# Optimization experiments

Measured on AMD Instinct MI355X. Metric: run time of the kernel, lower is better.

Reference implementation:

```python
import jax, jax.numpy as jnp
import numpy as np

NUM_EXPERTS = 8
CAPACITY_C = 1.0
ROUTER_TEMP = 1.0
EPS = 1e-10


def reference(x, router_w, router_b, w_gate, b_gate, w_up, b_up, w_down, b_down):
    # x: [B, S, H]
    B, S, H = x.shape
    n_tok = B * S
    k = int(n_tok * CAPACITY_C) // NUM_EXPERTS  # expert capacity (1024 here)

    xf = x.reshape(n_tok, H)  # (b s) h

    # Linear router (dropout p=0 -> identity), computed in float32 as in .float()
    clean_h = xf @ router_w + router_b  # [n_tok, E]

    # Gumbel noise (deterministic key stands in for torch.rand_like)
    u = jax.random.uniform(jax.random.key(42), clean_h.shape, dtype=clean_h.dtype)
    gumbel = -jnp.log(-jnp.log(u + EPS) + EPS)
    h = (clean_h + gumbel) / ROUTER_TEMP

    Sm = jax.nn.softmax(h, axis=-1)  # softmax over experts

    # top-k over the TOKEN dim (dim=0) per expert -> expert-choice routing
    Gt, idxt = jax.lax.top_k(Sm.T, k)  # [E, k]
    G = Gt.T            # [k, E] routing weights
    idx = idxt.T        # [k, E] chosen token indices

    # Gather routed tokens (replaces the one-hot einsum gather exactly:
    # top-k indices are distinct per expert, so one-hot matmul == take)
    toks = jnp.take(xf, idx, axis=0)  # [k, E, H]

    # Shared SwiGLU FFN (group_size=1 -> one expert instance reused E times)
    gate = jax.nn.silu(toks @ w_gate + b_gate)  # [k, E, dff]
    up = toks @ w_up + b_up                      # [k, E, dff]
    e_out = (gate * up) @ w_down + b_down        # [k, E, H]

    # Weight by G and scatter-add back to token positions, summed over experts
    weighted = G[..., None] * e_out              # [k, E, H]
    y = jnp.zeros_like(xf).at[idx.reshape(-1)].add(weighted.reshape(-1, H))
    return y.reshape(B, S, H)


def setup_inputs() -> dict:
    key = jax.random.key(0)
    ks = jax.random.split(key, 6)
    B, S, H, E = 4, 2048, 2048, NUM_EXPERTS
    dff = int(H * 4 * 2 / 3)  # 5461
    sH = 1.0 / np.sqrt(H)
    sF = 1.0 / np.sqrt(dff)
    return {
        "x": jax.random.normal(ks[0], (B, S, H), dtype=jnp.float32),
        "router_w": jax.random.normal(ks[1], (H, E), dtype=jnp.float32) * sH,
        "router_b": jnp.zeros((E,), dtype=jnp.float32),
        "w_gate": jax.random.normal(ks[2], (H, dff), dtype=jnp.float32) * sH,
        "b_gate": jnp.zeros((dff,), dtype=jnp.float32),
        "w_up": jax.random.normal(ks[3], (H, dff), dtype=jnp.float32) * sH,
        "b_up": jnp.zeros((dff,), dtype=jnp.float32),
        "w_down": jax.random.normal(ks[4], (dff, H), dtype=jnp.float32) * sF,
        "b_down": jnp.zeros((H,), dtype=jnp.float32),
    }
```

## Files before the change

kernel.cpp:

```cpp
#include <hip/hip_runtime.h>
#include <cstdint>
#include <cstddef>

#define N_TOK  8192
#define HDIM   2048
#define NEXP   8
#define KCAP   1024
#define DFF    5461
#define DFF_PB 5504
#define ACT_P  5504
#define NT1    (HDIM / 64)
#define NT2    (ACT_P / 64)

typedef unsigned short u16;
typedef short bf16x8 __attribute__((ext_vector_type(8)));
typedef float f32x4  __attribute__((ext_vector_type(4)));

__device__ __forceinline__ u16 f2bf(float f) {
  uint32_t u = __float_as_uint(f);
  uint32_t r = (u + 0x7FFFu + ((u >> 16) & 1u)) >> 16;
  return (u16)r;
}

__device__ __forceinline__ uint32_t rotl32(uint32_t v, int d) {
  return (v << d) | (v >> (32 - d));
}

__device__ uint32_t threefry_bits(uint32_t idx) {
  const uint32_t ks0 = 0u, ks1 = 42u, ks2 = 0u ^ 42u ^ 0x1BD11BDAu;
  uint32_t x0 = 0u + ks0;
  uint32_t x1 = idx + ks1;
#define TFR(d) { x0 += x1; x1 = rotl32(x1, d); x1 ^= x0; }
  TFR(13) TFR(15) TFR(26) TFR(6)
  x0 += ks1; x1 += ks2 + 1u;
  TFR(17) TFR(29) TFR(16) TFR(24)
  x0 += ks2; x1 += ks0 + 2u;
  TFR(13) TFR(15) TFR(26) TFR(6)
  x0 += ks0; x1 += ks1 + 3u;
  TFR(17) TFR(29) TFR(16) TFR(24)
  x0 += ks1; x1 += ks2 + 4u;
  TFR(13) TFR(15) TFR(26) TFR(6)
  x0 += ks2; x1 += ks0 + 5u;
#undef TFR
  return x0 ^ x1;
}

__global__ __launch_bounds__(256) void router_kernel(const float* __restrict__ x,
    const float* __restrict__ rw, const float* __restrict__ rb,
    float* __restrict__ SmT)
{
  const int lane = threadIdx.x & 63;
  const int wid  = threadIdx.x >> 6;
  const int t = blockIdx.x * 4 + wid;
  const float* xr = x + (size_t)t * HDIM;
  float acc[8] = {0.f,0.f,0.f,0.f,0.f,0.f,0.f,0.f};
#pragma unroll
  for (int it = 0; it < HDIM / 64; ++it) {
    int h = lane + it * 64;
    float xv = xr[h];
    const float4* wp = (const float4*)(rw + h * 8);
    float4 w0 = wp[0], w1 = wp[1];
    acc[0] = fmaf(xv, w0.x, acc[0]);
    acc[1] = fmaf(xv, w0.y, acc[1]);
    acc[2] = fmaf(xv, w0.z, acc[2]);
    acc[3] = fmaf(xv, w0.w, acc[3]);
    acc[4] = fmaf(xv, w1.x, acc[4]);
    acc[5] = fmaf(xv, w1.y, acc[5]);
    acc[6] = fmaf(xv, w1.z, acc[6]);
    acc[7] = fmaf(xv, w1.w, acc[7]);
  }
#pragma unroll
  for (int m = 32; m >= 1; m >>= 1) {
#pragma unroll
    for (int e = 0; e < 8; ++e) acc[e] += __shfl_xor(acc[e], m, 64);
  }
  if (lane == 0) {
    float h[8];
#pragma unroll
    for (int e = 0; e < 8; ++e) {
      uint32_t bits = threefry_bits((uint32_t)(t * 8 + e));
      float u = __uint_as_float((bits >> 9) | 0x3f800000u) - 1.0f;
      u = fmaxf(u, 0.0f);
      float g = -logf(-logf(u + 1e-10f) + 1e-10f);
      h[e] = acc[e] + rb[e] + g;
    }
    float mx = h[0];
#pragma unroll
    for (int e = 1; e < 8; ++e) mx = fmaxf(mx, h[e]);
    float ex[8]; float s = 0.f;
#pragma unroll
    for (int e = 0; e < 8; ++e) { ex[e] = expf(h[e] - mx); s += ex[e]; }
#pragma unroll
    for (int e = 0; e < 8; ++e) SmT[e * N_TOK + t] = ex[e] / s;
  }
}

__global__ __launch_bounds__(1024) void select_topk(const float* __restrict__ SmT,
    uint32_t* __restrict__ selTok, float* __restrict__ selW)
{
  const int e = blockIdx.x;
  const int tid = threadIdx.x;
  const float* v = SmT + (size_t)e * N_TOK;
  __shared__ uint32_t hist[256];
  __shared__ uint32_t sh_byte, sh_kk, sh_cnt, sh_eqc;
  uint32_t bitsv[8];
#pragma unroll
  for (int i = 0; i < 8; ++i) bitsv[i] = __float_as_uint(v[tid + i * 1024]);
  uint32_t prefix = 0;
  uint32_t kk = KCAP;
  for (int s = 3; s >= 0; --s) {
    if (tid < 256) hist[tid] = 0;
    __syncthreads();
    uint32_t himask = (s == 3) ? 0u : (0xFFFFFFFFu << ((s + 1) * 8));
#pragma unroll
    for (int i = 0; i < 8; ++i) {
      uint32_t b = bitsv[i];
      if ((b & himask) == prefix) atomicAdd(&hist[(b >> (s * 8)) & 255u], 1u);
    }
    __syncthreads();
    if (tid == 0) {
      uint32_t cum = 0; uint32_t bsel = 0, kn = kk;
      for (int b = 255; b >= 0; --b) {
        uint32_t c = hist[b];
        if (cum + c >= kk) { bsel = (uint32_t)b; kn = kk - cum; break; }
        cum += c;
      }
      sh_byte = bsel; sh_kk = kn;
    }
    __syncthreads();
    prefix |= sh_byte << (s * 8);
    kk = sh_kk;
  }
  const uint32_t T = prefix;
  const uint32_t need = kk;
  if (tid == 0) { sh_cnt = 0; sh_eqc = 0; }
  __syncthreads();
#pragma unroll
  for (int i = 0; i < 8; ++i) {
    uint32_t b = bitsv[i];
    if (b > T) {
      uint32_t p = atomicAdd(&sh_cnt, 1u);
      selTok[e * KCAP + p] = (uint32_t)(tid + i * 1024);
      selW[e * KCAP + p] = __uint_as_float(b);
    } else if (b == T) {
      atomicAdd(&sh_eqc, 1u);
    }
  }
  __syncthreads();
  if (sh_eqc == need) {
#pragma unroll
    for (int i = 0; i < 8; ++i) {
      if (bitsv[i] == T) {
        uint32_t p = atomicAdd(&sh_cnt, 1u);
        selTok[e * KCAP + p] = (uint32_t)(tid + i * 1024);
        selW[e * KCAP + p] = __uint_as_float(T);
      }
    }
  } else if (tid == 0) {
    uint32_t p = sh_cnt, rem = need;
    for (int t = 0; t < N_TOK && rem > 0u; ++t) {
      if (__float_as_uint(v[t]) == T) {
        selTok[e * KCAP + p] = (uint32_t)t;
        selW[e * KCAP + p] = __uint_as_float(T);
        ++p; --rem;
      }
    }
  }
}

__global__ __launch_bounds__(256) void build_inv(const uint32_t* __restrict__ selTok,
    int* __restrict__ inv)
{
  int s = blockIdx.x * 256 + threadIdx.x;
  inv[(s >> 10) * N_TOK + (int)selTok[s]] = s;
}

__global__ __launch_bounds__(256) void gather_kernel(const float* __restrict__ x,
    const uint32_t* __restrict__ selTok, u16* __restrict__ Xsel)
{
  const int slot = blockIdx.x;
  const int tid = threadIdx.x;
  const uint32_t tok = selTok[slot];
  const float4* src = (const float4*)(x + (size_t)tok * HDIM);
  float4 a = src[tid * 2], b = src[tid * 2 + 1];
  union { u16 h[8]; uint4 vv; } pk;
  pk.h[0] = f2bf(a.x); pk.h[1] = f2bf(a.y); pk.h[2] = f2bf(a.z); pk.h[3] = f2bf(a.w);
  pk.h[4] = f2bf(b.x); pk.h[5] = f2bf(b.y); pk.h[6] = f2bf(b.z); pk.h[7] = f2bf(b.w);
  ((uint4*)(Xsel + (size_t)slot * HDIM))[tid] = pk.vv;
}

__global__ __launch_bounds__(256) void transpose_convert(const float* __restrict__ in,
    int rows_in, int cols_in, u16* __restrict__ out, int out_cols)
{
  __shared__ float tile[32][33];
  const int bi = blockIdx.y;
  const int bj = blockIdx.x;
  const int tx = threadIdx.x, ty = threadIdx.y;
#pragma unroll
  for (int t = 0; t < 4; ++t) {
    int r = bi * 32 + ty + t * 8, c = bj * 32 + tx;
    float vv = (r < rows_in && c < cols_in) ? in[(size_t)r * cols_in + c] : 0.0f;
    tile[ty + t * 8][tx] = vv;
  }
  __syncthreads();
#pragma unroll
  for (int t = 0; t < 4; ++t) {
    int oj = bj * 32 + ty + t * 8;
    int oi = bi * 32 + tx;
    out[(size_t)oj * out_cols + oi] = f2bf(tile[tx][ty + t * 8]);
  }
}

#if defined(__has_builtin)
#  if __has_builtin(__builtin_amdgcn_global_load_lds)
#    define HAVE_GLD 1
#  endif
#endif
#ifdef HAVE_GLD
#define STG(gp, lp) __builtin_amdgcn_global_load_lds( \
    (const __attribute__((address_space(1))) void*)(gp), \
    (__attribute__((address_space(3))) void*)(lp), 16, 0, 0)
#define WAITV6() asm volatile("s_waitcnt vmcnt(6)" ::: "memory")
#define WAITV4() asm volatile("s_waitcnt vmcnt(4)" ::: "memory")
#define WAITV2() asm volatile("s_waitcnt vmcnt(2)" ::: "memory")
#define WAITV0() asm volatile("s_waitcnt vmcnt(0)" ::: "memory")
#else
#define STG(gp, lp) (*(bf16x8*)(lp) = *(const bf16x8*)(gp))
#define WAITV6() asm volatile("s_waitcnt vmcnt(0) lgkmcnt(0)" ::: "memory")
#define WAITV4() asm volatile("s_waitcnt vmcnt(0) lgkmcnt(0)" ::: "memory")
#define WAITV2() asm volatile("s_waitcnt vmcnt(0) lgkmcnt(0)" ::: "memory")
#define WAITV0() asm volatile("s_waitcnt vmcnt(0) lgkmcnt(0)" ::: "memory")
#endif
#define BAR()    __builtin_amdgcn_s_barrier()
#define SCHED0() __builtin_amdgcn_sched_barrier(0)
#define PRIO1()  __builtin_amdgcn_s_setprio(1)
#define PRIO0()  __builtin_amdgcn_s_setprio(0)
#define MFMA(a, b, c) __builtin_amdgcn_mfma_f32_16x16x32_bf16(a, b, c, 0, 0, 0)


__global__ __launch_bounds__(512, 2) void gemm1_kernel(
    const u16* __restrict__ Xsel,
    const u16* __restrict__ WgT,
    const u16* __restrict__ WuT,
    const float* __restrict__ bg, const float* __restrict__ bu,
    u16* __restrict__ act)
{
  __shared__ u16 AL[2][2][8192];
  __shared__ u16 GL[2][8192];
  __shared__ u16 UL[2][8192];

  const int id = blockIdx.x;
  const int xcd = id & 7;
  const int r = id >> 3;
  const int bm = xcd * 4 + (r & 3);
  const int bn = r >> 2;

  const int tid = threadIdx.x;
  const int lane = tid & 63, wid = tid >> 6;
  const int wm = wid >> 2, wn = wid & 3;
  const int fr = lane & 15, ck = lane >> 4;
  const int sw0 = (ck ^ (fr & 7)) * 8;
  const int sw1 = sw0 ^ 32;
  const int rA = (wm * 64 + fr) * 64;
  const int rB = (wn * 32 + fr) * 64;

  const int sr = tid >> 3;
  const int sq = (tid & 7) ^ (sr & 7);
  const u16* aS0 = Xsel + (size_t)(bm * 256 + sr) * HDIM + sq * 8;
  const u16* aS1 = aS0 + (size_t)128 * HDIM;
  const u16* gS  = WgT + (size_t)(bn * 128 + sr) * HDIM + sq * 8;
  const u16* uS  = WuT + (size_t)(bn * 128 + sr) * HDIM + sq * 8;

#define ST_A0(kt) { u16* d = &AL[(kt)&1][0][tid*8]; \
    STG(aS0 + (kt)*64, d); STG(aS0 + (kt)*64 + (size_t)64*HDIM, d + 4096); }
#define ST_A1(kt) { u16* d = &AL[(kt)&1][1][tid*8]; \
    STG(aS1 + (kt)*64, d); STG(aS1 + (kt)*64 + (size_t)64*HDIM, d + 4096); }
#define ST_G(kt) { u16* d = &GL[(kt)&1][tid*8]; \
    STG(gS + (kt)*64, d); STG(gS + (kt)*64 + (size_t)64*HDIM, d + 4096); }
#define ST_U(kt) { u16* d = &UL[(kt)&1][tid*8]; \
    STG(uS + (kt)*64, d); STG(uS + (kt)*64 + (size_t)64*HDIM, d + 4096); }

  f32x4 accg[8][2], accu[8][2];
  const f32x4 z4 = {0.f, 0.f, 0.f, 0.f};
#pragma unroll
  for (int i = 0; i < 8; ++i)
#pragma unroll
    for (int n = 0; n < 2; ++n) { accg[i][n] = z4; accu[i][n] = z4; }

  bf16x8 af[4][2], bgf[2][2], buf[2][2];

  ST_A0(0) ST_G(0) ST_U(0) ST_A1(0)
  WAITV4(); BAR(); SCHED0();

  for (int kt = 0; kt < NT1; ++kt) {
    const u16* A0 = AL[kt & 1][0];
    const u16* A1 = AL[kt & 1][1];
    const u16* G  = GL[kt & 1];
    const u16* U  = UL[kt & 1];
    const int st = (kt + 1 < NT1);
#pragma unroll
    for (int i = 0; i < 4; ++i) {
      af[i][0] = *(const bf16x8*)&A0[rA + i * 1024 + sw0];
      af[i][1] = *(const bf16x8*)&A0[rA + i * 1024 + sw1];
    }
#pragma unroll
    for (int n = 0; n < 2; ++n) {
      bgf[n][0] = *(const bf16x8*)&G[rB + n * 1024 + sw0];
      bgf[n][1] = *(const bf16x8*)&G[rB + n * 1024 + sw1];
    }
    if (st) ST_A0(kt + 1)
    PRIO1();
#pragma unroll
    for (int ks = 0; ks < 2; ++ks)
#pragma unroll
      for (int i = 0; i < 4; ++i)
#pragma unroll
        for (int n = 0; n < 2; ++n)
          accg[i][n] = MFMA(af[i][ks], bgf[n][ks], accg[i][n]);
    PRIO0();
    if (st) { WAITV4(); } else { WAITV2(); }
    BAR(); SCHED0();
#pragma unroll
    for (int n = 0; n < 2; ++n) {
      buf[n][0] = *(const bf16x8*)&U[rB + n * 1024 + sw0];
      buf[n][1] = *(const bf16x8*)&U[rB + n * 1024 + sw1];
    }
    if (st) { ST_G(kt + 1) ST_U(kt + 1) }
    PRIO1();
#pragma unroll
    for (int ks = 0; ks < 2; ++ks)
#pragma unroll
      for (int i = 0; i < 4; ++i)
#pragma unroll
        for (int n = 0; n < 2; ++n)
          accu[i][n] = MFMA(af[i][ks], buf[n][ks], accu[i][n]);
    PRIO0();
    if (st) { WAITV6(); } else { WAITV0(); }
    BAR(); SCHED0();
#pragma unroll
    for (int i = 0; i < 4; ++i) {
      af[i][0] = *(const bf16x8*)&A1[rA + i * 1024 + sw0];
      af[i][1] = *(const bf16x8*)&A1[rA + i * 1024 + sw1];
    }
    if (st) ST_A1(kt + 1)
    PRIO1();
#pragma unroll
    for (int ks = 0; ks < 2; ++ks)
#pragma unroll
      for (int i = 0; i < 4; ++i)
#pragma unroll
        for (int n = 0; n < 2; ++n) {
          accg[4 + i][n] = MFMA(af[i][ks], bgf[n][ks], accg[4 + i][n]);
          accu[4 + i][n] = MFMA(af[i][ks], buf[n][ks], accu[4 + i][n]);
        }
    PRIO0();
    WAITV4();
    BAR(); SCHED0();
  }

#pragma unroll
  for (int f = 0; f < 8; ++f) {
    const int rbase = bm * 256 + (f >> 2) * 128 + wm * 64 + (f & 3) * 16 + ck * 4;
#pragma unroll
    for (int v = 0; v < 4; ++v) {
      u16* arow = act + (size_t)(rbase + v) * ACT_P;
#pragma unroll
      for (int n = 0; n < 2; ++n) {
        const int col = bn * 128 + wn * 32 + n * 16 + fr;
        u16 ov = 0;
        if (col < DFF) {
          float gv = accg[f][n][v] + bg[col];
          float uv = accu[f][n][v] + bu[col];
          float e = __expf(-gv);
          float sv = gv * __builtin_amdgcn_rcpf(1.0f + e);
          ov = f2bf(sv * uv);
        }
        arow[col] = ov;
      }
    }
  }
#undef ST_A0
#undef ST_A1
#undef ST_G
#undef ST_U
}

__global__ __launch_bounds__(512, 2) void gemm2_kernel(
    const u16* __restrict__ act,
    const u16* __restrict__ WdT,
    const float* __restrict__ bd,
    const float* __restrict__ selW,
    float* __restrict__ Yslot)
{
  __shared__ u16 AL[2][2][8192];
  __shared__ u16 BL[2][2][8192];

  const int id = blockIdx.x;
  const int wg = (id & 7) * 32 + (id >> 3);
  const int bm = wg & 31, bn = wg >> 5;

  const int tid = threadIdx.x;
  const int lane = tid & 63, wid = tid >> 6;
  const int wm = wid >> 2, wn = wid & 3;
  const int fr = lane & 15, ck = lane >> 4;
  const int sw0 = (ck ^ (fr & 7)) * 8;
  const int sw1 = sw0 ^ 32;
  const int rA = (wm * 64 + fr) * 64;
  const int rB = (wn * 32 + fr) * 64;

  const int sr = tid >> 3;
  const int sq = (tid & 7) ^ (sr & 7);
  const u16* aS0 = act + (size_t)(bm * 256 + sr) * ACT_P + sq * 8;
  const u16* aS1 = aS0 + (size_t)128 * ACT_P;
  const u16* bS0 = WdT + (size_t)(bn * 256 + sr) * ACT_P + sq * 8;
  const u16* bS1 = bS0 + (size_t)128 * ACT_P;

#define ST_A0(kt) { u16* d = &AL[(kt)&1][0][tid*8]; \
    STG(aS0 + (kt)*64, d); STG(aS0 + (kt)*64 + (size_t)64*ACT_P, d + 4096); }
#define ST_A1(kt) { u16* d = &AL[(kt)&1][1][tid*8]; \
    STG(aS1 + (kt)*64, d); STG(aS1 + (kt)*64 + (size_t)64*ACT_P, d + 4096); }
#define ST_B0(kt) { u16* d = &BL[(kt)&1][0][tid*8]; \
    STG(bS0 + (kt)*64, d); STG(bS0 + (kt)*64 + (size_t)64*ACT_P, d + 4096); }
#define ST_B1(kt) { u16* d = &BL[(kt)&1][1][tid*8]; \
    STG(bS1 + (kt)*64, d); STG(bS1 + (kt)*64 + (size_t)64*ACT_P, d + 4096); }

  f32x4 acc[8][4];
  const f32x4 z4 = {0.f, 0.f, 0.f, 0.f};
#pragma unroll
  for (int i = 0; i < 8; ++i)
#pragma unroll
    for (int n = 0; n < 4; ++n) acc[i][n] = z4;

  bf16x8 af[4][2], b0[2][2], b1[2][2];

  ST_A0(0) ST_B0(0) ST_B1(0) ST_A1(0)
  WAITV4(); BAR(); SCHED0();

  for (int kt = 0; kt < NT2; ++kt) {
    const u16* A0 = AL[kt & 1][0];
    const u16* A1 = AL[kt & 1][1];
    const u16* B0 = BL[kt & 1][0];
    const u16* B1 = BL[kt & 1][1];
    const int st = (kt + 1 < NT2);
#pragma unroll
    for (int i = 0; i < 4; ++i) {
      af[i][0] = *(const bf16x8*)&A0[rA + i * 1024 + sw0];
      af[i][1] = *(const bf16x8*)&A0[rA + i * 1024 + sw1];
    }
#pragma unroll
    for (int n = 0; n < 2; ++n) {
      b0[n][0] = *(const bf16x8*)&B0[rB + n * 1024 + sw0];
      b0[n][1] = *(const bf16x8*)&B0[rB + n * 1024 + sw1];
    }
    if (st) ST_A0(kt + 1)
    PRIO1();
#pragma unroll
    for (int ks = 0; ks < 2; ++ks)
#pragma unroll
      for (int i = 0; i < 4; ++i)
#pragma unroll
        for (int n = 0; n < 2; ++n)
          acc[i][n] = MFMA(af[i][ks], b0[n][ks], acc[i][n]);
    PRIO0();
    if (st) { WAITV4(); } else { WAITV2(); }
    BAR(); SCHED0();
#pragma unroll
    for (int n = 0; n < 2; ++n) {
      b1[n][0] = *(const bf16x8*)&B1[rB + n * 1024 + sw0];
      b1[n][1] = *(const bf16x8*)&B1[rB + n * 1024 + sw1];
    }
    if (st) { ST_B0(kt + 1) ST_B1(kt + 1) }
    PRIO1();
#pragma unroll
    for (int ks = 0; ks < 2; ++ks)
#pragma unroll
      for (int i = 0; i < 4; ++i)
#pragma unroll
        for (int n = 0; n < 2; ++n)
          acc[i][2 + n] = MFMA(af[i][ks], b1[n][ks], acc[i][2 + n]);
    PRIO0();
    if (st) { WAITV6(); } else { WAITV0(); }
    BAR(); SCHED0();
#pragma unroll
    for (int i = 0; i < 4; ++i) {
      af[i][0] = *(const bf16x8*)&A1[rA + i * 1024 + sw0];
      af[i][1] = *(const bf16x8*)&A1[rA + i * 1024 + sw1];
    }
    if (st) ST_A1(kt + 1)
    PRIO1();
#pragma unroll
    for (int ks = 0; ks < 2; ++ks)
#pragma unroll
      for (int i = 0; i < 4; ++i)
#pragma unroll
        for (int n = 0; n < 2; ++n) {
          acc[4 + i][n]     = MFMA(af[i][ks], b0[n][ks], acc[4 + i][n]);
          acc[4 + i][2 + n] = MFMA(af[i][ks], b1[n][ks], acc[4 + i][2 + n]);
        }
    PRIO0();
    WAITV4();
    BAR(); SCHED0();
  }

#pragma unroll
  for (int f = 0; f < 8; ++f) {
    const int rbase = bm * 256 + (f >> 2) * 128 + wm * 64 + (f & 3) * 16 + ck * 4;
#pragma unroll
    for (int v = 0; v < 4; ++v) {
      const int srow = rbase + v;
      const float w = selW[srow];
      float* yrow = Yslot + (size_t)srow * HDIM;
#pragma unroll
      for (int n = 0; n < 4; ++n) {
        const int col = bn * 256 + (n >> 1) * 128 + wn * 32 + (n & 1) * 16 + fr;
        yrow[col] = w * (acc[f][n][v] + bd[col]);
      }
    }
  }
#undef ST_A0
#undef ST_A1
#undef ST_B0
#undef ST_B1
}

__global__ __launch_bounds__(256) void scatter_kernel(const float* __restrict__ Yslot,
    const int* __restrict__ inv, float* __restrict__ y)
{
  const int t = blockIdx.x;
  const int c = threadIdx.x * 8;
  float4 a0 = {0.f,0.f,0.f,0.f}, a1 = {0.f,0.f,0.f,0.f};
#pragma unroll
  for (int e = 0; e < 8; ++e) {
    const int s = inv[e * N_TOK + t];
    if (s >= 0) {
      const float4* p = (const float4*)(Yslot + (size_t)s * HDIM + c);
      float4 v0 = p[0], v1 = p[1];
      a0.x += v0.x; a0.y += v0.y; a0.z += v0.z; a0.w += v0.w;
      a1.x += v1.x; a1.y += v1.y; a1.z += v1.z; a1.w += v1.w;
    }
  }
  float4* yp = (float4*)(y + (size_t)t * HDIM + c);
  yp[0] = a0; yp[1] = a1;
}

extern "C" void kernel_launch(void* const* d_in, const int* in_sizes, int n_in,
                              void* d_out, int out_size, void* d_ws, size_t ws_size,
                              hipStream_t stream) {
  const float* x      = (const float*)d_in[0];
  const float* rw     = (const float*)d_in[1];
  const float* rb     = (const float*)d_in[2];
  const float* w_gate = (const float*)d_in[3];
  const float* b_gate = (const float*)d_in[4];
  const float* w_up   = (const float*)d_in[5];
  const float* b_up   = (const float*)d_in[6];
  const float* w_down = (const float*)d_in[7];
  const float* b_down = (const float*)d_in[8];
  float* y = (float*)d_out;

  uint8_t* ws = (uint8_t*)d_ws;
  uint32_t* selTok = (uint32_t*)(ws + 0);
  float*    selW   = (float*)(ws + 32768);
  int*      inv    = (int*)(ws + 65536);
  u16*      act    = (u16*)(ws + 327680);
  u16*      Xsel   = (u16*)(ws + 90505216ull);
  u16*      WdT    = (u16*)(ws + 90505216ull);
  float*    Yslot  = (float*)(ws + 113049600ull);
  float*    SmT    = (float*)(ws + 124059648ull);
  u16*      WgT    = (u16*)(ws + 124321792ull);
  u16*      WuT    = (u16*)(ws + 146866176ull);

  hipMemsetAsync(inv, 0xFF, NEXP * N_TOK * sizeof(int), stream);
  transpose_convert<<<dim3(172, 64), dim3(32, 8), 0, stream>>>(w_gate, 2048, DFF, WgT, 2048);
  transpose_convert<<<dim3(172, 64), dim3(32, 8), 0, stream>>>(w_up,   2048, DFF, WuT, 2048);
  router_kernel<<<N_TOK / 4, 256, 0, stream>>>(x, rw, rb, SmT);
  select_topk<<<NEXP, 1024, 0, stream>>>(SmT, selTok, selW);
  build_inv<<<N_TOK / 256, 256, 0, stream>>>(selTok, inv);
  gather_kernel<<<N_TOK, 256, 0, stream>>>(x, selTok, Xsel);
  gemm1_kernel<<<43 * 32, 512, 0, stream>>>(Xsel, WgT, WuT, b_gate, b_up, act);
  transpose_convert<<<dim3(64, 172), dim3(32, 8), 0, stream>>>(w_down, DFF, 2048, WdT, ACT_P);
  gemm2_kernel<<<8 * 32, 512, 0, stream>>>(act, WdT, b_down, selW, Yslot);
  scatter_kernel<<<N_TOK, 256, 0, stream>>>(Yslot, inv, y);
}
```

Baseline: 874.7 us.

## Add LDS-fragment barriers in GEMM main loops and fold inverse map into top-k

Inserts an extra barrier plus an explicit LDS wait (lgkmcnt) after each fragment-read phase in both GEMM main loops. The apparent aim is to keep waves in lockstep so the MFMA bursts line up and global-to-LDS staging overlaps better. It also writes the inverse token-to-slot map directly inside select_topk, which removes the separate build_inv kernel launch. The extra barriers per K step add synchronisation cost and could stall waves that would otherwise run ahead.

Result: no change. 891.4 us (+1.9%).

```diff
diff --git a/kernel.cpp b/kernel.cpp
--- a/kernel.cpp
+++ b/kernel.cpp
@@ -96,7 +96,7 @@
 }
 
 __global__ __launch_bounds__(1024) void select_topk(const float* __restrict__ SmT,
-    uint32_t* __restrict__ selTok, float* __restrict__ selW)
+    uint32_t* __restrict__ selTok, float* __restrict__ selW, int* __restrict__ inv)
 {
   const int e = blockIdx.x;
   const int tid = threadIdx.x;
@@ -140,8 +140,10 @@
     uint32_t b = bitsv[i];
     if (b > T) {
       uint32_t p = atomicAdd(&sh_cnt, 1u);
-      selTok[e * KCAP + p] = (uint32_t)(tid + i * 1024);
+      const uint32_t tok = (uint32_t)(tid + i * 1024);
+      selTok[e * KCAP + p] = tok;
       selW[e * KCAP + p] = __uint_as_float(b);
+      inv[e * N_TOK + tok] = (int)(e * KCAP + p);
     } else if (b == T) {
       atomicAdd(&sh_eqc, 1u);
     }
@@ -152,8 +154,10 @@
     for (int i = 0; i < 8; ++i) {
       if (bitsv[i] == T) {
         uint32_t p = atomicAdd(&sh_cnt, 1u);
-        selTok[e * KCAP + p] = (uint32_t)(tid + i * 1024);
+        const uint32_t tok = (uint32_t)(tid + i * 1024);
+        selTok[e * KCAP + p] = tok;
         selW[e * KCAP + p] = __uint_as_float(T);
+        inv[e * N_TOK + tok] = (int)(e * KCAP + p);
       }
     }
   } else if (tid == 0) {
@@ -162,17 +166,11 @@
       if (__float_as_uint(v[t]) == T) {
         selTok[e * KCAP + p] = (uint32_t)t;
         selW[e * KCAP + p] = __uint_as_float(T);
+        inv[e * N_TOK + t] = (int)(e * KCAP + p);
         ++p; --rem;
       }
     }
   }
-}
-
-__global__ __launch_bounds__(256) void build_inv(const uint32_t* __restrict__ selTok,
-    int* __restrict__ inv)
-{
-  int s = blockIdx.x * 256 + threadIdx.x;
-  inv[(s >> 10) * N_TOK + (int)selTok[s]] = s;
 }
 
 __global__ __launch_bounds__(256) void gather_kernel(const float* __restrict__ x,
@@ -231,6 +229,8 @@
 #define WAITV2() asm volatile("s_waitcnt vmcnt(0) lgkmcnt(0)" ::: "memory")
 #define WAITV0() asm volatile("s_waitcnt vmcnt(0) lgkmcnt(0)" ::: "memory")
 #endif
+#define WAITLGKM0() asm volatile("s_waitcnt lgkmcnt(0)" ::: "memory")
+#define WAITLGKM8() asm volatile("s_waitcnt lgkmcnt(8)" ::: "memory")
 #define BAR()    __builtin_amdgcn_s_barrier()
 #define SCHED0() __builtin_amdgcn_sched_barrier(0)
 #define PRIO1()  __builtin_amdgcn_s_setprio(1)
@@ -309,6 +309,9 @@
       bgf[n][1] = *(const bf16x8*)&G[rB + n * 1024 + sw1];
     }
     if (st) ST_A0(kt + 1)
+    WAITLGKM8();
+    BAR();
+    WAITLGKM0(); SCHED0();
     PRIO1();
 #pragma unroll
     for (int ks = 0; ks < 2; ++ks)
@@ -326,6 +329,8 @@
       buf[n][1] = *(const bf16x8*)&U[rB + n * 1024 + sw1];
     }
     if (st) { ST_G(kt + 1) ST_U(kt + 1) }
+    BAR();
+    WAITLGKM0(); SCHED0();
     PRIO1();
 #pragma unroll
     for (int ks = 0; ks < 2; ++ks)
@@ -343,6 +348,8 @@
       af[i][1] = *(const bf16x8*)&A1[rA + i * 1024 + sw1];
     }
     if (st) ST_A1(kt + 1)
+    BAR();
+    WAITLGKM0(); SCHED0();
     PRIO1();
 #pragma unroll
     for (int ks = 0; ks < 2; ++ks)
@@ -453,6 +460,9 @@
       b0[n][1] = *(const bf16x8*)&B0[rB + n * 1024 + sw1];
     }
     if (st) ST_A0(kt + 1)
+    WAITLGKM8();
+    BAR();
+    WAITLGKM0(); SCHED0();
     PRIO1();
 #pragma unroll
     for (int ks = 0; ks < 2; ++ks)
@@ -470,6 +480,8 @@
       b1[n][1] = *(const bf16x8*)&B1[rB + n * 1024 + sw1];
     }
     if (st) { ST_B0(kt + 1) ST_B1(kt + 1) }
+    BAR();
+    WAITLGKM0(); SCHED0();
     PRIO1();
 #pragma unroll
     for (int ks = 0; ks < 2; ++ks)
@@ -487,6 +499,8 @@
       af[i][1] = *(const bf16x8*)&A1[rA + i * 1024 + sw1];
     }
     if (st) ST_A1(kt + 1)
+    BAR();
+    WAITLGKM0(); SCHED0();
     PRIO1();
 #pragma unroll
     for (int ks = 0; ks < 2; ++ks)
@@ -573,8 +587,7 @@
   transpose_convert<<<dim3(172, 64), dim3(32, 8), 0, stream>>>(w_gate, 2048, DFF, WgT, 2048);
   transpose_convert<<<dim3(172, 64), dim3(32, 8), 0, stream>>>(w_up,   2048, DFF, WuT, 2048);
   router_kernel<<<N_TOK / 4, 256, 0, stream>>>(x, rw, rb, SmT);
-  select_topk<<<NEXP, 1024, 0, stream>>>(SmT, selTok, selW);
-  build_inv<<<N_TOK / 256, 256, 0, stream>>>(selTok, inv);
+  select_topk<<<NEXP, 1024, 0, stream>>>(SmT, selTok, selW, inv);
   gather_kernel<<<N_TOK, 256, 0, stream>>>(x, selTok, Xsel);
   gemm1_kernel<<<43 * 32, 512, 0, stream>>>(Xsel, WgT, WuT, b_gate, b_up, act);
   transpose_convert<<<dim3(64, 172), dim3(32, 8), 0, stream>>>(w_down, DFF, 2048, WdT, ACT_P);
```
